# Optimization experiments

Measured on AMD Instinct MI355X. Metric: run time of the kernel, lower is better.

Reference implementation:

```python
import jax, jax.numpy as jnp
import numpy as np

EMBED = 1024
HEADS = 16


def setup_inputs() -> dict:
    key = jax.random.key(0)
    ks = jax.random.split(key, 7)
    scale = 1.0 / np.sqrt(EMBED)
    x = jax.random.normal(ks[0], (4, 2048, EMBED), dtype=jnp.float32)
    Wq = jax.random.normal(ks[1], (EMBED, EMBED), dtype=jnp.float32) * scale
    bq = jax.random.normal(ks[2], (EMBED,), dtype=jnp.float32) * 0.01
    Wk = jax.random.normal(ks[3], (EMBED, EMBED), dtype=jnp.float32) * scale
    bk = jax.random.normal(ks[4], (EMBED,), dtype=jnp.float32) * 0.01
    Wv = jax.random.normal(ks[5], (EMBED, EMBED), dtype=jnp.float32) * scale
    bv = jax.random.normal(ks[6], (EMBED,), dtype=jnp.float32) * 0.01
    return {"x": x, "Wq": Wq, "bq": bq, "Wk": Wk, "bk": bk, "Wv": Wv, "bv": bv}


def reference(x, Wq, bq, Wk, bk, Wv, bv):
    b, s, n = x.shape
    h = HEADS
    d = n // h
    # torch nn.Linear: y = x @ W.T + b
    q = (jnp.einsum("bsn,mn->bsm", x, Wq) + bq).reshape(b, s, h, d).transpose(0, 2, 1, 3)
    k = (jnp.einsum("bsn,mn->bsm", x, Wk) + bk).reshape(b, s, h, d).transpose(0, 2, 1, 3)
    v = (jnp.einsum("bsn,mn->bsm", x, Wv) + bv).reshape(b, s, h, d).transpose(0, 2, 1, 3)
    # scores: [b, h, s_q, s_k]; fixed scale of 1/10 as in the source
    scores = jnp.einsum("bhqd,bhkd->bhqk", q, k) / 10.0
    # NOTE: softmax over dim=-2 (the QUERY axis), matching the source exactly
    attn = jax.nn.softmax(scores, axis=-2)
    out = jnp.einsum("bhqk,bhkd->bhqd", attn, v)
    return out.transpose(0, 2, 1, 3).reshape(b, s, n)
```

## Files before the change

### kernel.cpp

```cpp
#include <hip/hip_runtime.h>
#include <math.h>

#define SEQ    2048
#define EMBED  1024
#define HEADS  16
#define HDIM   64
#define BATCH  4
#define ROWS   (BATCH * SEQ)
#define BH     (BATCH * HEADS)

typedef _Float16 f16;
typedef __attribute__((ext_vector_type(8))) _Float16 f16x8;
typedef __attribute__((ext_vector_type(4))) _Float16 f16x4;
typedef __attribute__((ext_vector_type(4))) float    f32x4;

__device__ __forceinline__ void async16(void* l, const void* g) {
    __builtin_amdgcn_global_load_lds(
        (__attribute__((address_space(1))) void*)(uintptr_t)g,
        (__attribute__((address_space(3))) void*)(uint32_t)(uintptr_t)l,
        16, 0, 0);
}
__device__ __forceinline__ void async4(void* l, const void* g) {
    __builtin_amdgcn_global_load_lds(
        (__attribute__((address_space(1))) void*)(uintptr_t)g,
        (__attribute__((address_space(3))) void*)(uint32_t)(uintptr_t)l,
        4, 0, 0);
}

__device__ __forceinline__ f32x4 mfma16(f16x8 a, f16x8 b, f32x4 c) {
    return __builtin_amdgcn_mfma_f32_16x16x32_f16(a, b, c, 0, 0, 0);
}

#define NX4 (ROWS * EMBED / 4)
#define NW4 (EMBED * EMBED / 4)
__global__ __launch_bounds__(256) void cvt_kernel(
    const float* __restrict__ x,
    const float* __restrict__ Wq, const float* __restrict__ Wk,
    const float* __restrict__ Wv,
    f16* __restrict__ xh, f16* __restrict__ Wh)
{
    int i = blockIdx.x * 256 + threadIdx.x;
    const float4* src; f16* dst; int j;
    if (i < NX4)              { src = (const float4*)x;  dst = xh;                j = i; }
    else if (i < NX4 + NW4)   { src = (const float4*)Wq; dst = Wh;                j = i - NX4; }
    else if (i < NX4 + 2*NW4) { src = (const float4*)Wk; dst = Wh + EMBED*EMBED;  j = i - NX4 - NW4; }
    else                      { src = (const float4*)Wv; dst = Wh + 2*EMBED*EMBED;j = i - NX4 - 2*NW4; }
    float4 v = src[j];
    f16x4 h;
    h[0] = (f16)v.x; h[1] = (f16)v.y; h[2] = (f16)v.z; h[3] = (f16)v.w;
    *(f16x4*)(dst + (size_t)j * 4) = h;
}

__global__ __launch_bounds__(256) void proj_kernel(
    const f16* __restrict__ A,
    const f16* __restrict__ W,
    const float* __restrict__ bq, const float* __restrict__ bk,
    const float* __restrict__ bv,
    f16* __restrict__ Qh, f16* __restrict__ Kh, f16* __restrict__ Vt)
{
    __shared__ f16 As[128 * 32];
    __shared__ f16 Bs[128 * 32];

    const int t = threadIdx.x, wv = t >> 6, lane = t & 63;
    const int lm = lane & 15, quad = lane >> 4;
    const int r0 = blockIdx.x * 128, c0 = blockIdx.y * 128;
    const int wm = wv & 1, wn = wv >> 1;

    const int srow = wv * 32 + (lane >> 2);
    const int sch  = (lane & 3) * 8;
    const f16* gA = A + (size_t)(r0 + srow) * EMBED + sch;
    const f16* gB = W + (size_t)(c0 + srow) * EMBED + sch;
    f16* lA = As + wv * 1024;
    f16* lB = Bs + wv * 1024;

    f32x4 acc[4][4];
#pragma unroll
    for (int i = 0; i < 4; ++i)
#pragma unroll
        for (int j = 0; j < 4; ++j) acc[i][j] = (f32x4){0.f, 0.f, 0.f, 0.f};

    for (int kk = 0; kk < EMBED; kk += 32) {
        __syncthreads();
        async16(lA,        gA + kk);
        async16(lA + 512,  gA + 16 * EMBED + kk);
        async16(lB,        gB + kk);
        async16(lB + 512,  gB + 16 * EMBED + kk);
        __syncthreads();

        f16x8 af[4], bf[4];
#pragma unroll
        for (int i = 0; i < 4; ++i)
            af[i] = *(const f16x8*)&As[(wm * 64 + i * 16 + lm) * 32 + quad * 8];
#pragma unroll
        for (int i = 0; i < 4; ++i)
            bf[i] = *(const f16x8*)&Bs[(wn * 64 + i * 16 + lm) * 32 + quad * 8];
#pragma unroll
        for (int mi = 0; mi < 4; ++mi)
#pragma unroll
            for (int ni = 0; ni < 4; ++ni)
                acc[mi][ni] = mfma16(af[mi], bf[ni], acc[mi][ni]);
    }

    const int z = c0 >> 10;
    const float* bias = (z == 0) ? bq : (z == 1) ? bk : bv;
#pragma unroll
    for (int ni = 0; ni < 4; ++ni) {
        int col = c0 + wn * 64 + ni * 16 + lm;
        int cz  = col & 1023;
        float bb = bias[cz];
        int h = cz >> 6, d = cz & 63;
#pragma unroll
        for (int mi = 0; mi < 4; ++mi) {
            int rbase = r0 + wm * 64 + mi * 16 + quad * 4;
            int b = rbase >> 11, s = rbase & 2047;
            if (z < 2) {
                f16* O = (z == 0) ? Qh : Kh;
                size_t base = ((size_t)(b * HEADS + h) * SEQ + s) * HDIM + d;
#pragma unroll
                for (int r = 0; r < 4; ++r)
                    O[base + (size_t)r * HDIM] = (f16)(acc[mi][ni][r] + bb);
            } else {
                f16x4 pk;
#pragma unroll
                for (int r = 0; r < 4; ++r) pk[r] = (f16)(acc[mi][ni][r] + bb);
                *(f16x4*)&Vt[((size_t)(b * HEADS + h) * HDIM + d) * SEQ + s] = pk;
            }
        }
    }
}

__global__ __launch_bounds__(256) void stats_kernel(
    const f16* __restrict__ Qh, const f16* __restrict__ Kh,
    float* __restrict__ linv)
{
    __shared__ f16 Ks[128 * 64];
    __shared__ f16 Qs[64 * 64];

    const int t = threadIdx.x, wv = t >> 6, lane = t & 63;
    const int lm = lane & 15, quad = lane >> 4;
    const int bh = blockIdx.y, k0 = blockIdx.x * 128;
    const int grow = lane >> 3, gch = (lane & 7) * 8;
    const size_t base = (size_t)bh * SEQ * HDIM;

#pragma unroll
    for (int i = 0; i < 4; ++i) {
        int g = wv * 4 + i;
        async16(Ks + g * 512, Kh + base + (size_t)(k0 + g * 8 + grow) * HDIM + gch);
    }
    __syncthreads();

    f16x8 kf[2][2];
#pragma unroll
    for (int ct = 0; ct < 2; ++ct)
#pragma unroll
        for (int ds = 0; ds < 2; ++ds)
            kf[ct][ds] = *(const f16x8*)&Ks[(wv * 32 + ct * 16 + lm) * 64 + ds * 32 + quad * 8];

    float cs0 = 0.f, cs1 = 0.f;
    for (int q0 = 0; q0 < SEQ; q0 += 64) {
        __syncthreads();
#pragma unroll
        for (int i = 0; i < 2; ++i) {
            int g = wv * 2 + i;
            async16(Qs + g * 512, Qh + base + (size_t)(q0 + g * 8 + grow) * HDIM + gch);
        }
        __syncthreads();
#pragma unroll
        for (int qt = 0; qt < 4; ++qt) {
            f16x8 a0 = *(const f16x8*)&Qs[(qt * 16 + lm) * 64 + quad * 8];
            f16x8 a1 = *(const f16x8*)&Qs[(qt * 16 + lm) * 64 + 32 + quad * 8];
            f32x4 c0v = (f32x4){0.f, 0.f, 0.f, 0.f};
            f32x4 c1v = (f32x4){0.f, 0.f, 0.f, 0.f};
            c0v = mfma16(a0, kf[0][0], c0v); c0v = mfma16(a1, kf[0][1], c0v);
            c1v = mfma16(a0, kf[1][0], c1v); c1v = mfma16(a1, kf[1][1], c1v);
#pragma unroll
            for (int r = 0; r < 4; ++r) {
                cs0 += __expf(c0v[r] * 0.1f);
                cs1 += __expf(c1v[r] * 0.1f);
            }
        }
    }
    cs0 += __shfl_xor(cs0, 16, 64); cs0 += __shfl_xor(cs0, 32, 64);
    cs1 += __shfl_xor(cs1, 16, 64); cs1 += __shfl_xor(cs1, 32, 64);
    if (quad == 0) {
        linv[(size_t)bh * SEQ + k0 + wv * 32 + lm]      = 1.0f / cs0;
        linv[(size_t)bh * SEQ + k0 + wv * 32 + 16 + lm] = 1.0f / cs1;
    }
}

__global__ __launch_bounds__(256) void out_kernel(
    const f16* __restrict__ Qh, const f16* __restrict__ Kh,
    const f16* __restrict__ Vt, const float* __restrict__ linv,
    float* __restrict__ out)
{
    __shared__ f16 Ps[4 * 32 * 72];
    __shared__ f16 Ks[64 * 64];
    __shared__ f16 Vs[64 * 64];
    __shared__ float Ls[64];

    const int t = threadIdx.x, wv = t >> 6, lane = t & 63;
    const int lm = lane & 15, quad = lane >> 4;
    const int bh = blockIdx.y, q0 = blockIdx.x * 128;
    const int b = bh >> 4, h = bh & 15;
    const int grow = lane >> 3, gch = (lane & 7) * 8;
    const size_t base = (size_t)bh * SEQ * HDIM;

#pragma unroll
    for (int i = 0; i < 4; ++i) {
        int g = wv * 4 + i;
        async16(Ps + g * 512, Qh + base + (size_t)(q0 + g * 8 + grow) * HDIM + gch);
    }
    __syncthreads();
    f16x8 qa[2][2];
#pragma unroll
    for (int qs = 0; qs < 2; ++qs)
#pragma unroll
        for (int ds = 0; ds < 2; ++ds)
            qa[qs][ds] = *(const f16x8*)&Ps[(wv * 32 + qs * 16 + lm) * 64 + ds * 32 + quad * 8];

    f32x4 oacc[2][4];
#pragma unroll
    for (int i = 0; i < 2; ++i)
#pragma unroll
        for (int j = 0; j < 4; ++j) oacc[i][j] = (f32x4){0.f, 0.f, 0.f, 0.f};

    f16* Pw = Ps + wv * (32 * 72);

    for (int k0 = 0; k0 < SEQ; k0 += 64) {
        __syncthreads();
#pragma unroll
        for (int i = 0; i < 2; ++i) {
            int g = wv * 2 + i;
            async16(Ks + g * 512, Kh + base + (size_t)(k0 + g * 8 + grow) * HDIM + gch);
            async16(Vs + g * 512, Vt + base + (size_t)(g * 8 + grow) * SEQ + k0 + gch);
        }
        if (wv == 0) async4(Ls, linv + (size_t)bh * SEQ + k0 + lane);
        __syncthreads();

#pragma unroll
        for (int ct = 0; ct < 4; ++ct) {
            f16x8 kf0 = *(const f16x8*)&Ks[(ct * 16 + lm) * 64 + quad * 8];
            f16x8 kf1 = *(const f16x8*)&Ks[(ct * 16 + lm) * 64 + 32 + quad * 8];
            float li[4];
#pragma unroll
            for (int r = 0; r < 4; ++r) li[r] = Ls[ct * 16 + quad * 4 + r] * 1024.0f;
#pragma unroll
            for (int qs = 0; qs < 2; ++qs) {
                f32x4 s4 = (f32x4){0.f, 0.f, 0.f, 0.f};
                s4 = mfma16(kf0, qa[qs][0], s4);
                s4 = mfma16(kf1, qa[qs][1], s4);
                f16x4 pk;
#pragma unroll
                for (int r = 0; r < 4; ++r)
                    pk[r] = (f16)(__expf(s4[r] * 0.1f) * li[r]);
                *(f16x4*)&Pw[(qs * 16 + lm) * 72 + ct * 16 + quad * 4] = pk;
            }
        }
#pragma unroll
        for (int ks = 0; ks < 2; ++ks) {
            f16x8 pa0 = *(const f16x8*)&Pw[(lm) * 72 + ks * 32 + quad * 8];
            f16x8 pa1 = *(const f16x8*)&Pw[(16 + lm) * 72 + ks * 32 + quad * 8];
#pragma unroll
            for (int dt = 0; dt < 4; ++dt) {
                f16x8 vb = *(const f16x8*)&Vs[(dt * 16 + lm) * 64 + ks * 32 + quad * 8];
                oacc[0][dt] = mfma16(pa0, vb, oacc[0][dt]);
                oacc[1][dt] = mfma16(pa1, vb, oacc[1][dt]);
            }
        }
    }

    const float inv1024 = 1.0f / 1024.0f;
#pragma unroll
    for (int qt = 0; qt < 2; ++qt)
#pragma unroll
        for (int dt = 0; dt < 4; ++dt) {
            int col = h * HDIM + dt * 16 + lm;
#pragma unroll
            for (int r = 0; r < 4; ++r) {
                int s = q0 + wv * 32 + qt * 16 + quad * 4 + r;
                out[((size_t)b * SEQ + s) * EMBED + col] = oacc[qt][dt][r] * inv1024;
            }
        }
}

extern "C" void kernel_launch(void* const* d_in, const int* in_sizes, int n_in,
                              void* d_out, int out_size, void* d_ws, size_t ws_size,
                              hipStream_t stream) {
    const float* x  = (const float*)d_in[0];
    const float* Wq = (const float*)d_in[1];
    const float* bq = (const float*)d_in[2];
    const float* Wk = (const float*)d_in[3];
    const float* bk = (const float*)d_in[4];
    const float* Wv = (const float*)d_in[5];
    const float* bv = (const float*)d_in[6];
    float* out = (float*)d_out;

    f16* xh = (f16*)d_ws;
    f16* Wh = xh + (size_t)ROWS * EMBED;
    f16* Qh = Wh + (size_t)3 * EMBED * EMBED;
    f16* Kh = Qh + (size_t)BH * SEQ * HDIM;
    f16* Vt = Kh + (size_t)BH * SEQ * HDIM;
    float* linv = (float*)(Vt + (size_t)BH * SEQ * HDIM);

    cvt_kernel<<<(NX4 + 3 * NW4) / 256, 256, 0, stream>>>(x, Wq, Wk, Wv, xh, Wh);
    proj_kernel<<<dim3(ROWS / 128, 3 * EMBED / 128), 256, 0, stream>>>(
        xh, Wh, bq, bk, bv, Qh, Kh, Vt);
    stats_kernel<<<dim3(SEQ / 128, BH), 256, 0, stream>>>(Qh, Kh, linv);
    out_kernel<<<dim3(SEQ / 128, BH), 256, 0, stream>>>(Qh, Kh, Vt, linv, out);
}
```

Baseline: 340.1 us.

## Use 32x32 MFMA, swizzled LDS, fold column normalizer into V

The attention kernels move to 32x32x16 MFMA tiles with 256-row blocks and XOR-swizzled LDS layouts to avoid bank conflicts. The stats kernel now scales V in place by the per-key inverse column sum, so the output kernel no longer loads or applies linv. exp is computed via exp2f and packed with cvt_pkrtz, and the proj kernel stages the V transpose through LDS for coalesced stores. Storing the scaled normalizer and scaled V in fp16 may reduce accuracy, and the larger blocks halve the number of attention workgroups.

```diff
diff --git a/kernel.cpp b/kernel.cpp
--- a/kernel.cpp
+++ b/kernel.cpp
@@ -10,9 +10,13 @@
 #define BH     (BATCH * HEADS)
 
 typedef _Float16 f16;
+typedef __attribute__((ext_vector_type(2))) _Float16 f16x2;
+typedef __attribute__((ext_vector_type(4))) _Float16 f16x4;
 typedef __attribute__((ext_vector_type(8))) _Float16 f16x8;
-typedef __attribute__((ext_vector_type(4))) _Float16 f16x4;
-typedef __attribute__((ext_vector_type(4))) float    f32x4;
+typedef __attribute__((ext_vector_type(4)))  float   f32x4;
+typedef __attribute__((ext_vector_type(16))) float   f32x16;
+
+#define EXP2C 0.14426950408889634f
 
 __device__ __forceinline__ void async16(void* l, const void* g) {
     __builtin_amdgcn_global_load_lds(
@@ -20,15 +24,28 @@
         (__attribute__((address_space(3))) void*)(uint32_t)(uintptr_t)l,
         16, 0, 0);
 }
-__device__ __forceinline__ void async4(void* l, const void* g) {
-    __builtin_amdgcn_global_load_lds(
-        (__attribute__((address_space(1))) void*)(uintptr_t)g,
-        (__attribute__((address_space(3))) void*)(uint32_t)(uintptr_t)l,
-        4, 0, 0);
-}
-
 __device__ __forceinline__ f32x4 mfma16(f16x8 a, f16x8 b, f32x4 c) {
     return __builtin_amdgcn_mfma_f32_16x16x32_f16(a, b, c, 0, 0, 0);
+}
+__device__ __forceinline__ f32x16 mfma32(f16x8 a, f16x8 b, f32x16 c) {
+    return __builtin_amdgcn_mfma_f32_32x32x16_f16(a, b, c, 0, 0, 0);
+}
+__device__ __forceinline__ f32x16 zero16() {
+    f32x16 z;
+#pragma unroll
+    for (int i = 0; i < 16; ++i) z[i] = 0.f;
+    return z;
+}
+__device__ __forceinline__ f16x2 pk2(float a, float b) {
+    union {
+        __fp16 __attribute__((ext_vector_type(2))) h;
+        f16x2 f;
+    } u;
+    u.h = __builtin_amdgcn_cvt_pkrtz(a, b);
+    return u.f;
+}
+__device__ __forceinline__ int swz64(int row, int gran) {
+    return row * 64 + ((gran ^ (row & 7)) << 3);
 }
 
 #define NX4 (ROWS * EMBED / 4)
@@ -60,16 +77,17 @@
 {
     __shared__ f16 As[128 * 32];
     __shared__ f16 Bs[128 * 32];
+    __shared__ f16 Ts[64 * 132];
 
     const int t = threadIdx.x, wv = t >> 6, lane = t & 63;
     const int lm = lane & 15, quad = lane >> 4;
     const int r0 = blockIdx.x * 128, c0 = blockIdx.y * 128;
     const int wm = wv & 1, wn = wv >> 1;
 
-    const int srow = wv * 32 + (lane >> 2);
-    const int sch  = (lane & 3) * 8;
-    const f16* gA = A + (size_t)(r0 + srow) * EMBED + sch;
-    const f16* gB = W + (size_t)(c0 + srow) * EMBED + sch;
+    const int srow = lane >> 2;
+    const int sgr  = (lane & 3) ^ (srow & 3);
+    const f16* gA = A + (size_t)(r0 + wv * 32 + srow) * EMBED + sgr * 8;
+    const f16* gB = W + (size_t)(c0 + wv * 32 + srow) * EMBED + sgr * 8;
     f16* lA = As + wv * 1024;
     f16* lB = Bs + wv * 1024;
 
@@ -82,18 +100,22 @@
     for (int kk = 0; kk < EMBED; kk += 32) {
         __syncthreads();
         async16(lA,        gA + kk);
-        async16(lA + 512,  gA + 16 * EMBED + kk);
+        async16(lA + 512,  gA + (size_t)16 * EMBED + kk);
         async16(lB,        gB + kk);
-        async16(lB + 512,  gB + 16 * EMBED + kk);
+        async16(lB + 512,  gB + (size_t)16 * EMBED + kk);
         __syncthreads();
 
         f16x8 af[4], bf[4];
 #pragma unroll
-        for (int i = 0; i < 4; ++i)
-            af[i] = *(const f16x8*)&As[(wm * 64 + i * 16 + lm) * 32 + quad * 8];
-#pragma unroll
-        for (int i = 0; i < 4; ++i)
-            bf[i] = *(const f16x8*)&Bs[(wn * 64 + i * 16 + lm) * 32 + quad * 8];
+        for (int i = 0; i < 4; ++i) {
+            int row = wm * 64 + i * 16 + lm;
+            af[i] = *(const f16x8*)&As[row * 32 + ((quad ^ (row & 3)) << 3)];
+        }
+#pragma unroll
+        for (int i = 0; i < 4; ++i) {
+            int row = wn * 64 + i * 16 + lm;
+            bf[i] = *(const f16x8*)&Bs[row * 32 + ((quad ^ (row & 3)) << 3)];
+        }
 #pragma unroll
         for (int mi = 0; mi < 4; ++mi)
 #pragma unroll
@@ -103,27 +125,53 @@
 
     const int z = c0 >> 10;
     const float* bias = (z == 0) ? bq : (z == 1) ? bk : bv;
-#pragma unroll
-    for (int ni = 0; ni < 4; ++ni) {
-        int col = c0 + wn * 64 + ni * 16 + lm;
-        int cz  = col & 1023;
-        float bb = bias[cz];
-        int h = cz >> 6, d = cz & 63;
-#pragma unroll
-        for (int mi = 0; mi < 4; ++mi) {
-            int rbase = r0 + wm * 64 + mi * 16 + quad * 4;
-            int b = rbase >> 11, s = rbase & 2047;
-            if (z < 2) {
-                f16* O = (z == 0) ? Qh : Kh;
+    const int b  = r0 >> 11;
+    const int s0 = r0 & 2047;
+
+    if (z < 2) {
+        f16* O = (z == 0) ? Qh : Kh;
+#pragma unroll
+        for (int ni = 0; ni < 4; ++ni) {
+            int cz = (c0 & 1023) + wn * 64 + ni * 16 + lm;
+            float bb = bias[cz];
+            int h = cz >> 6, d = cz & 63;
+#pragma unroll
+            for (int mi = 0; mi < 4; ++mi) {
+                int s = s0 + wm * 64 + mi * 16 + quad * 4;
                 size_t base = ((size_t)(b * HEADS + h) * SEQ + s) * HDIM + d;
 #pragma unroll
                 for (int r = 0; r < 4; ++r)
                     O[base + (size_t)r * HDIM] = (f16)(acc[mi][ni][r] + bb);
-            } else {
-                f16x4 pk;
-#pragma unroll
-                for (int r = 0; r < 4; ++r) pk[r] = (f16)(acc[mi][ni][r] + bb);
-                *(f16x4*)&Vt[((size_t)(b * HEADS + h) * HDIM + d) * SEQ + s] = pk;
+            }
+        }
+    } else {
+#pragma unroll 1
+        for (int hd = 0; hd < 2; ++hd) {
+            __syncthreads();
+            if (wn == hd) {
+#pragma unroll
+                for (int ni = 0; ni < 4; ++ni) {
+                    int cz = (c0 & 1023) + wn * 64 + ni * 16 + lm;
+                    float bb = bias[cz];
+                    int dloc = ni * 16 + lm;
+#pragma unroll
+                    for (int mi = 0; mi < 4; ++mi) {
+                        int sloc = wm * 64 + mi * 16 + quad * 4;
+                        f16x4 pk;
+#pragma unroll
+                        for (int r = 0; r < 4; ++r) pk[r] = (f16)(acc[mi][ni][r] + bb);
+                        *(f16x4*)&Ts[dloc * 132 + sloc] = pk;
+                    }
+                }
+            }
+            __syncthreads();
+            int hout = ((c0 & 1023) >> 6) + hd;
+            int dl = t >> 2, soff = (t & 3) * 32;
+            size_t gbase = ((size_t)(b * HEADS + hout) * HDIM + dl) * SEQ + s0 + soff;
+#pragma unroll
+            for (int c = 0; c < 8; ++c) {
+                f16x4 v = *(const f16x4*)&Ts[dl * 132 + soff + 4 * c];
+                *(f16x4*)&Vt[gbase + 4 * c] = v;
             }
         }
     }
@@ -131,154 +179,189 @@
 
 __global__ __launch_bounds__(256) void stats_kernel(
     const f16* __restrict__ Qh, const f16* __restrict__ Kh,
-    float* __restrict__ linv)
+    f16* __restrict__ Vt)
 {
-    __shared__ f16 Ks[128 * 64];
+    __shared__ f16 Kst[256 * 64];
     __shared__ f16 Qs[64 * 64];
+    __shared__ f16 Ls[256];
 
     const int t = threadIdx.x, wv = t >> 6, lane = t & 63;
-    const int lm = lane & 15, quad = lane >> 4;
-    const int bh = blockIdx.y, k0 = blockIdx.x * 128;
-    const int grow = lane >> 3, gch = (lane & 7) * 8;
-    const size_t base = (size_t)bh * SEQ * HDIM;
-
-#pragma unroll
-    for (int i = 0; i < 4; ++i) {
-        int g = wv * 4 + i;
-        async16(Ks + g * 512, Kh + base + (size_t)(k0 + g * 8 + grow) * HDIM + gch);
+    const int lm = lane & 31, half = lane >> 5;
+    const int bh = blockIdx.y, k0 = blockIdx.x * 256;
+    const size_t base  = (size_t)bh * SEQ * HDIM;
+    const size_t vbase = (size_t)bh * HDIM * SEQ;
+
+    const int srow = lane >> 3;
+    const int sgr  = (lane & 7) ^ (srow & 7);
+
+#pragma unroll
+    for (int i = 0; i < 8; ++i) {
+        int rr = wv * 64 + 8 * i;
+        async16(Kst + rr * 64,
+                Kh + base + (size_t)(k0 + rr + srow) * 64 + sgr * 8);
     }
     __syncthreads();
 
-    f16x8 kf[2][2];
-#pragma unroll
-    for (int ct = 0; ct < 2; ++ct)
-#pragma unroll
-        for (int ds = 0; ds < 2; ++ds)
-            kf[ct][ds] = *(const f16x8*)&Ks[(wv * 32 + ct * 16 + lm) * 64 + ds * 32 + quad * 8];
+    f16x8 Kf[2][4];
+#pragma unroll
+    for (int kt = 0; kt < 2; ++kt)
+#pragma unroll
+        for (int kg = 0; kg < 4; ++kg)
+            Kf[kt][kg] = *(const f16x8*)&Kst[swz64(wv * 64 + kt * 32 + lm, 2 * kg + half)];
 
     float cs0 = 0.f, cs1 = 0.f;
     for (int q0 = 0; q0 < SEQ; q0 += 64) {
         __syncthreads();
 #pragma unroll
         for (int i = 0; i < 2; ++i) {
-            int g = wv * 2 + i;
-            async16(Qs + g * 512, Qh + base + (size_t)(q0 + g * 8 + grow) * HDIM + gch);
-        }
-        __syncthreads();
-#pragma unroll
-        for (int qt = 0; qt < 4; ++qt) {
-            f16x8 a0 = *(const f16x8*)&Qs[(qt * 16 + lm) * 64 + quad * 8];
-            f16x8 a1 = *(const f16x8*)&Qs[(qt * 16 + lm) * 64 + 32 + quad * 8];
-            f32x4 c0v = (f32x4){0.f, 0.f, 0.f, 0.f};
-            f32x4 c1v = (f32x4){0.f, 0.f, 0.f, 0.f};
-            c0v = mfma16(a0, kf[0][0], c0v); c0v = mfma16(a1, kf[0][1], c0v);
-            c1v = mfma16(a0, kf[1][0], c1v); c1v = mfma16(a1, kf[1][1], c1v);
-#pragma unroll
-            for (int r = 0; r < 4; ++r) {
-                cs0 += __expf(c0v[r] * 0.1f);
-                cs1 += __expf(c1v[r] * 0.1f);
-            }
-        }
-    }
-    cs0 += __shfl_xor(cs0, 16, 64); cs0 += __shfl_xor(cs0, 32, 64);
-    cs1 += __shfl_xor(cs1, 16, 64); cs1 += __shfl_xor(cs1, 32, 64);
-    if (quad == 0) {
-        linv[(size_t)bh * SEQ + k0 + wv * 32 + lm]      = 1.0f / cs0;
-        linv[(size_t)bh * SEQ + k0 + wv * 32 + 16 + lm] = 1.0f / cs1;
+            int rr = wv * 16 + 8 * i;
+            async16(Qs + rr * 64,
+                    Qh + base + (size_t)(q0 + rr + srow) * 64 + sgr * 8);
+        }
+        __syncthreads();
+#pragma unroll
+        for (int qt = 0; qt < 2; ++qt) {
+            f16x8 Qf[4];
+#pragma unroll
+            for (int kg = 0; kg < 4; ++kg)
+                Qf[kg] = *(const f16x8*)&Qs[swz64(qt * 32 + lm, 2 * kg + half)];
+            f32x16 s0v = zero16(), s1v = zero16();
+#pragma unroll
+            for (int kg = 0; kg < 4; ++kg) {
+                s0v = mfma32(Qf[kg], Kf[0][kg], s0v);
+                s1v = mfma32(Qf[kg], Kf[1][kg], s1v);
+            }
+#pragma unroll
+            for (int e = 0; e < 16; ++e) {
+                cs0 += exp2f(s0v[e] * EXP2C);
+                cs1 += exp2f(s1v[e] * EXP2C);
+            }
+        }
+    }
+    cs0 += __shfl_xor(cs0, 32, 64);
+    cs1 += __shfl_xor(cs1, 32, 64);
+    if (half == 0) {
+        Ls[wv * 64 + lm]      = (f16)(64.0f / cs0);
+        Ls[wv * 64 + 32 + lm] = (f16)(64.0f / cs1);
+    }
+    __syncthreads();
+
+    {
+        int dl = t >> 2, koff = (t & 3) * 64;
+        size_t g = vbase + (size_t)dl * SEQ + k0 + koff;
+#pragma unroll
+        for (int c = 0; c < 8; ++c) {
+            f16x8 v  = *(const f16x8*)&Vt[g + 8 * c];
+            f16x8 lv = *(const f16x8*)&Ls[koff + 8 * c];
+            v = v * lv;
+            *(f16x8*)&Vt[g + 8 * c] = v;
+        }
     }
 }
 
 __global__ __launch_bounds__(256) void out_kernel(
     const f16* __restrict__ Qh, const f16* __restrict__ Kh,
-    const f16* __restrict__ Vt, const float* __restrict__ linv,
-    float* __restrict__ out)
+    const f16* __restrict__ Vt, float* __restrict__ out)
 {
-    __shared__ f16 Ps[4 * 32 * 72];
+    __shared__ f16 Qs[256 * 64];
     __shared__ f16 Ks[64 * 64];
     __shared__ f16 Vs[64 * 64];
-    __shared__ float Ls[64];
 
     const int t = threadIdx.x, wv = t >> 6, lane = t & 63;
-    const int lm = lane & 15, quad = lane >> 4;
-    const int bh = blockIdx.y, q0 = blockIdx.x * 128;
+    const int lm = lane & 31, half = lane >> 5;
+    const int bh = blockIdx.y, q0 = blockIdx.x * 256;
     const int b = bh >> 4, h = bh & 15;
-    const int grow = lane >> 3, gch = (lane & 7) * 8;
-    const size_t base = (size_t)bh * SEQ * HDIM;
-
-#pragma unroll
-    for (int i = 0; i < 4; ++i) {
-        int g = wv * 4 + i;
-        async16(Ps + g * 512, Qh + base + (size_t)(q0 + g * 8 + grow) * HDIM + gch);
+    const size_t base  = (size_t)bh * SEQ * HDIM;
+    const size_t vbase = (size_t)bh * HDIM * SEQ;
+
+    const int srow = lane >> 3;
+    const int sgr  = (lane & 7) ^ (srow & 7);
+
+#pragma unroll
+    for (int i = 0; i < 8; ++i) {
+        int rr = wv * 64 + 8 * i;
+        async16(Qs + rr * 64,
+                Qh + base + (size_t)(q0 + rr + srow) * 64 + sgr * 8);
     }
     __syncthreads();
-    f16x8 qa[2][2];
-#pragma unroll
-    for (int qs = 0; qs < 2; ++qs)
-#pragma unroll
-        for (int ds = 0; ds < 2; ++ds)
-            qa[qs][ds] = *(const f16x8*)&Ps[(wv * 32 + qs * 16 + lm) * 64 + ds * 32 + quad * 8];
-
-    f32x4 oacc[2][4];
+
+    f16x8 Qf[2][4];
+#pragma unroll
+    for (int qt = 0; qt < 2; ++qt)
+#pragma unroll
+        for (int kg = 0; kg < 4; ++kg)
+            Qf[qt][kg] = *(const f16x8*)&Qs[swz64(wv * 64 + qt * 32 + lm, 2 * kg + half)];
+
+    f32x16 oacc[2][2];
 #pragma unroll
     for (int i = 0; i < 2; ++i)
 #pragma unroll
-        for (int j = 0; j < 4; ++j) oacc[i][j] = (f32x4){0.f, 0.f, 0.f, 0.f};
-
-    f16* Pw = Ps + wv * (32 * 72);
+        for (int j = 0; j < 2; ++j) oacc[i][j] = zero16();
+
+    f16* Pw = Qs + wv * 64 * 64;
 
     for (int k0 = 0; k0 < SEQ; k0 += 64) {
         __syncthreads();
 #pragma unroll
         for (int i = 0; i < 2; ++i) {
-            int g = wv * 2 + i;
-            async16(Ks + g * 512, Kh + base + (size_t)(k0 + g * 8 + grow) * HDIM + gch);
-            async16(Vs + g * 512, Vt + base + (size_t)(g * 8 + grow) * SEQ + k0 + gch);
-        }
-        if (wv == 0) async4(Ls, linv + (size_t)bh * SEQ + k0 + lane);
-        __syncthreads();
-
-#pragma unroll
-        for (int ct = 0; ct < 4; ++ct) {
-            f16x8 kf0 = *(const f16x8*)&Ks[(ct * 16 + lm) * 64 + quad * 8];
-            f16x8 kf1 = *(const f16x8*)&Ks[(ct * 16 + lm) * 64 + 32 + quad * 8];
-            float li[4];
-#pragma unroll
-            for (int r = 0; r < 4; ++r) li[r] = Ls[ct * 16 + quad * 4 + r] * 1024.0f;
-#pragma unroll
-            for (int qs = 0; qs < 2; ++qs) {
-                f32x4 s4 = (f32x4){0.f, 0.f, 0.f, 0.f};
-                s4 = mfma16(kf0, qa[qs][0], s4);
-                s4 = mfma16(kf1, qa[qs][1], s4);
-                f16x4 pk;
-#pragma unroll
-                for (int r = 0; r < 4; ++r)
-                    pk[r] = (f16)(__expf(s4[r] * 0.1f) * li[r]);
-                *(f16x4*)&Pw[(qs * 16 + lm) * 72 + ct * 16 + quad * 4] = pk;
-            }
-        }
-#pragma unroll
-        for (int ks = 0; ks < 2; ++ks) {
-            f16x8 pa0 = *(const f16x8*)&Pw[(lm) * 72 + ks * 32 + quad * 8];
-            f16x8 pa1 = *(const f16x8*)&Pw[(16 + lm) * 72 + ks * 32 + quad * 8];
-#pragma unroll
-            for (int dt = 0; dt < 4; ++dt) {
-                f16x8 vb = *(const f16x8*)&Vs[(dt * 16 + lm) * 64 + ks * 32 + quad * 8];
-                oacc[0][dt] = mfma16(pa0, vb, oacc[0][dt]);
-                oacc[1][dt] = mfma16(pa1, vb, oacc[1][dt]);
-            }
-        }
-    }
-
-    const float inv1024 = 1.0f / 1024.0f;
+            int rr = wv * 16 + 8 * i;
+            async16(Ks + rr * 64,
+                    Kh + base + (size_t)(k0 + rr + srow) * 64 + sgr * 8);
+            async16(Vs + rr * 64,
+                    Vt + vbase + (size_t)(rr + srow) * SEQ + k0 + sgr * 8);
+        }
+        __syncthreads();
+
+#pragma unroll
+        for (int kt = 0; kt < 2; ++kt) {
+            f16x8 Kfr[4];
+#pragma unroll
+            for (int kg = 0; kg < 4; ++kg)
+                Kfr[kg] = *(const f16x8*)&Ks[swz64(kt * 32 + lm, 2 * kg + half)];
+#pragma unroll
+            for (int qt = 0; qt < 2; ++qt) {
+                f32x16 st = zero16();
+#pragma unroll
+                for (int kg = 0; kg < 4; ++kg)
+                    st = mfma32(Kfr[kg], Qf[qt][kg], st);
+                int row = qt * 32 + lm;
+#pragma unroll
+                for (int g = 0; g < 4; ++g) {
+                    union { f16x2 h2[2]; f16x4 h4; } u;
+                    u.h2[0] = pk2(exp2f(st[4*g+0] * EXP2C), exp2f(st[4*g+1] * EXP2C));
+                    u.h2[1] = pk2(exp2f(st[4*g+2] * EXP2C), exp2f(st[4*g+3] * EXP2C));
+                    *(f16x4*)&Pw[row * 64 + (((4*kt+g) ^ (row & 7)) << 3) + half * 4] = u.h4;
+                }
+            }
+        }
+
+        f16x8 Vf[2][4];
+#pragma unroll
+        for (int dt = 0; dt < 2; ++dt)
+#pragma unroll
+            for (int kc = 0; kc < 4; ++kc)
+                Vf[dt][kc] = *(const f16x8*)&Vs[swz64(dt * 32 + lm, 2 * kc + half)];
+#pragma unroll
+        for (int qt = 0; qt < 2; ++qt) {
+            int row = qt * 32 + lm;
+#pragma unroll
+            for (int kc = 0; kc < 4; ++kc) {
+                f16x8 Pf = *(const f16x8*)&Pw[row * 64 + (((2*kc+half) ^ (row & 7)) << 3)];
+                oacc[qt][0] = mfma32(Pf, Vf[0][kc], oacc[qt][0]);
+                oacc[qt][1] = mfma32(Pf, Vf[1][kc], oacc[qt][1]);
+            }
+        }
+    }
+
 #pragma unroll
     for (int qt = 0; qt < 2; ++qt)
 #pragma unroll
-        for (int dt = 0; dt < 4; ++dt) {
-            int col = h * HDIM + dt * 16 + lm;
-#pragma unroll
-            for (int r = 0; r < 4; ++r) {
-                int s = q0 + wv * 32 + qt * 16 + quad * 4 + r;
-                out[((size_t)b * SEQ + s) * EMBED + col] = oacc[qt][dt][r] * inv1024;
+        for (int dt = 0; dt < 2; ++dt) {
+            int col = h * HDIM + dt * 32 + lm;
+#pragma unroll
+            for (int e = 0; e < 16; ++e) {
+                int s = q0 + wv * 64 + qt * 32 + (e & 3) + 8 * (e >> 2) + 4 * half;
+                out[((size_t)b * SEQ + s) * EMBED + col] = oacc[qt][dt][e] * 0.015625f;
             }
         }
 }
@@ -300,11 +383,10 @@
     f16* Qh = Wh + (size_t)3 * EMBED * EMBED;
     f16* Kh = Qh + (size_t)BH * SEQ * HDIM;
     f16* Vt = Kh + (size_t)BH * SEQ * HDIM;
-    float* linv = (float*)(Vt + (size_t)BH * SEQ * HDIM);
 
     cvt_kernel<<<(NX4 + 3 * NW4) / 256, 256, 0, stream>>>(x, Wq, Wk, Wv, xh, Wh);
     proj_kernel<<<dim3(ROWS / 128, 3 * EMBED / 128), 256, 0, stream>>>(
         xh, Wh, bq, bk, bv, Qh, Kh, Vt);
-    stats_kernel<<<dim3(SEQ / 128, BH), 256, 0, stream>>>(Qh, Kh, linv);
-    out_kernel<<<dim3(SEQ / 128, BH), 256, 0, stream>>>(Qh, Kh, Vt, linv, out);
-}
+    stats_kernel<<<dim3(SEQ / 256, BH), 256, 0, stream>>>(Qh, Kh, Vt);
+    out_kernel<<<dim3(SEQ / 256, BH), 256, 0, stream>>>(Qh, Kh, Vt, out);
+}
```

After: 370.2 us. 1.09x slower.
